# Kernel tuning notes

Measured on AMD Instinct MI355X. Metric: run time of the kernel, lower is better.

Reference implementation:

```python
import jax, jax.numpy as jnp
import numpy as np

D_MANIFOLD = 1024
D_FIBER = 512


def setup_inputs() -> dict:
    key = jax.random.key(0)
    ks = jax.random.split(key, 9)
    B, SQ, SK = 4, 4096, 4096
    m_states = jax.random.normal(ks[0], (B, SQ, D_MANIFOLD), dtype=jnp.float32)
    f_states_k = jax.random.normal(ks[1], (B, SK, D_FIBER), dtype=jnp.float32)
    f_states_v = jax.random.normal(ks[2], (B, SK, D_FIBER), dtype=jnp.float32)
    s_q = 1.0 / np.sqrt(D_MANIFOLD)
    s_f = 1.0 / np.sqrt(D_FIBER)
    W_q = jax.random.uniform(ks[3], (D_MANIFOLD, D_FIBER), jnp.float32, -s_q, s_q)
    b_q = jax.random.uniform(ks[4], (D_FIBER,), jnp.float32, -s_q, s_q)
    W_k = jax.random.uniform(ks[5], (D_FIBER, D_FIBER), jnp.float32, -s_f, s_f)
    b_k = jax.random.uniform(ks[6], (D_FIBER,), jnp.float32, -s_f, s_f)
    W_v = jax.random.uniform(ks[7], (D_FIBER, D_FIBER), jnp.float32, -s_f, s_f)
    b_v = jax.random.uniform(ks[8], (D_FIBER,), jnp.float32, -s_f, s_f)
    return {
        "m_states": m_states,
        "f_states_k": f_states_k,
        "f_states_v": f_states_v,
        "W_q": W_q, "b_q": b_q,
        "W_k": W_k, "b_k": b_k,
        "W_v": W_v, "b_v": b_v,
    }


def reference(m_states, f_states_k, f_states_v, W_q, b_q, W_k, b_k, W_v, b_v):
    scale = D_FIBER ** (-0.5)
    Q = jnp.einsum("bsm,md->bsd", m_states, W_q) + b_q   # [B,SQ,Df]
    K = jnp.einsum("btf,fd->btd", f_states_k, W_k) + b_k  # [B,SK,Df]
    V = jnp.einsum("btf,fd->btd", f_states_v, W_v) + b_v  # [B,SK,Df]
    scores = jnp.einsum("bsd,btd->bst", Q, K) * scale     # [B,SQ,SK]
    weights = jax.nn.softmax(scores, axis=-1)
    return jnp.einsum("bst,btd->bsd", weights, V)         # [B,SQ,Df]
```

## Files before the change

### kernel.cpp

```cpp
#include <hip/hip_runtime.h>


typedef __attribute__((ext_vector_type(8)))  short short8;
typedef __attribute__((ext_vector_type(16))) float f32x16;
typedef __attribute__((ext_vector_type(4)))  float float4v;

__device__ __forceinline__ short f2bf(float x){
  unsigned int u = __float_as_uint(x);
  u = (u + 0x7FFFu + ((u >> 16) & 1u)) >> 16;
  return (short)u;
}

__device__ __forceinline__ unsigned cvt_pk_bf16(float a, float b){
  unsigned r;
  asm("v_cvt_pk_bf16_f32 %0, %1, %2" : "=v"(r) : "v"(a), "v"(b));
  return r;
}

__device__ __forceinline__ float fast_exp2(float x){
  float r; asm("v_exp_f32 %0, %1" : "=v"(r) : "v"(x)); return r;
}

__device__ __forceinline__ void bar_lgkm(){
  asm volatile("s_waitcnt lgkmcnt(0)" ::: "memory");
  __builtin_amdgcn_s_barrier();
}

typedef const __attribute__((address_space(1))) unsigned int guint_t;
typedef __attribute__((address_space(3))) unsigned int luint_t;
__device__ __forceinline__ void gl_lds16(const void* g, void* l){
  __builtin_amdgcn_global_load_lds((guint_t*)g, (luint_t*)l, 16, 0, 0);
}

__global__ __launch_bounds__(256) void transpose_cvt_fused(
    const float* __restrict__ Wq, const float* __restrict__ Wk,
    const float* __restrict__ Wv,
    short* __restrict__ WqT, short* __restrict__ WkT, short* __restrict__ WvT)
{
  int idx = blockIdx.x * 256 + threadIdx.x;
  if (idx < 524288){
    int n = idx & 511, k = idx >> 9;
    WqT[(n<<10) + k] = f2bf(Wq[idx]);
  } else if (idx < 786432){
    int j = idx - 524288; int n = j & 511, k = j >> 9;
    WkT[(n<<9) + k] = f2bf(Wk[j]);
  } else {
    int j = idx - 786432; int n = j & 511, k = j >> 9;
    WvT[(n<<9) + k] = f2bf(Wv[j]);
  }
}

__global__ __launch_bounds__(256, 2) void proj_gemm_fused(
    const float* __restrict__ Aq, const float* __restrict__ Ak,
    const float* __restrict__ Av,
    const short* __restrict__ Wq, const short* __restrict__ Wk,
    const short* __restrict__ Wv,
    const float* __restrict__ bq, const float* __restrict__ bk,
    const float* __restrict__ bv,
    short* __restrict__ Cq, short* __restrict__ Ck, short* __restrict__ Cv,
    float scale)
{
  __shared__ char As[8192];
  __shared__ char Bs[65536];
  const int pz = blockIdx.y;
  const float* A    = (pz==0) ? Aq : (pz==1) ? Ak : Av;
  const short* WT   = (pz==0) ? Wq : (pz==1) ? Wk : Wv;
  const float* bias = (pz==0) ? bq : (pz==1) ? bk : bv;
  short* C          = (pz==0) ? Cq : (pz==1) ? Ck : Cv;
  const int K       = (pz==0) ? 1024 : 512;
  const float alpha = (pz==0) ? scale : 1.0f;

  const int tid = threadIdx.x;
  const int wid = tid >> 6, lane = tid & 63;
  const int lo = lane & 31, hi = lane >> 5;
  const int bm = blockIdx.x;
  const char* WTb = (const char*)WT;

  f32x16 acc[2][4];
  #pragma unroll
  for (int i=0;i<2;i++)
    #pragma unroll
    for (int j=0;j<4;j++)
      #pragma unroll
      for (int r=0;r<16;r++) acc[i][j][r] = 0.0f;

  const int srow = tid >> 2, sslot = tid & 3;
  for (int k0 = 0; k0 < K; k0 += 64) {
    #pragma unroll
    for (int i=0;i<16;i++){
      const int rb0 = wid*128 + i*8;
      const int rr = lane >> 3;
      const void* src = WTb + ((size_t)(rb0 + rr)*K + k0)*2
                        + (((lane&7)*16) ^ (rr<<4));
      gl_lds16(src, Bs + rb0*128);
    }
    {
      const float4v* src = (const float4v*)&A[(size_t)(bm*64+srow)*K + k0 + sslot*16];
      float4v f0 = src[0], f1 = src[1], f2 = src[2], f3 = src[3];
      uint4 u0, u1;
      u0.x = cvt_pk_bf16(f0[0], f0[1]);
      u0.y = cvt_pk_bf16(f0[2], f0[3]);
      u0.z = cvt_pk_bf16(f1[0], f1[1]);
      u0.w = cvt_pk_bf16(f1[2], f1[3]);
      u1.x = cvt_pk_bf16(f2[0], f2[1]);
      u1.y = cvt_pk_bf16(f2[2], f2[3]);
      u1.z = cvt_pk_bf16(f3[0], f3[1]);
      u1.w = cvt_pk_bf16(f3[2], f3[3]);
      const int swz = (srow&7)<<4;
      *(uint4*)(As + srow*128 + ((sslot*32)      ^ swz)) = u0;
      *(uint4*)(As + srow*128 + ((sslot*32 + 16) ^ swz)) = u1;
    }
    __syncthreads();
    #pragma unroll
    for (int dc=0; dc<4; dc++){
      short8 af[2], bfr[4];
      #pragma unroll
      for (int mt=0;mt<2;mt++){
        const int ra = mt*32+lo;
        af[mt] = *(const short8*)(As + ra*128 + ((dc*32 + hi*16) ^ ((ra&7)<<4)));
      }
      #pragma unroll
      for (int nt=0;nt<4;nt++){
        const int rb = wid*128 + nt*32 + lo;
        bfr[nt] = *(const short8*)(Bs + rb*128 + ((dc*32 + hi*16) ^ ((rb&7)<<4)));
      }
      #pragma unroll
      for (int mt=0;mt<2;mt++)
        #pragma unroll
        for (int nt=0;nt<4;nt++)
          acc[mt][nt] = __builtin_amdgcn_mfma_f32_32x32x16_bf16(af[mt], bfr[nt], acc[mt][nt], 0, 0, 0);
    }
    __syncthreads();
  }

  char* Cb = (char*)C;
  #pragma unroll
  for (int nt=0;nt<4;nt++){
    const int col = wid*128 + nt*32 + lo;
    const float bv2 = bias[col];
    #pragma unroll
    for (int mt=0;mt<2;mt++){
      const int grow0 = bm*64 + mt*32;
      if (pz == 0){
        #pragma unroll
        for (int r=0;r<16;r++){
          const int t = grow0 + (r&3) + 8*(r>>2) + 4*hi;
          const int d = col;
          const float val = (acc[mt][nt][r] + bv2) * alpha;
          size_t addr = (size_t)(t>>6)*65536
                      + (size_t)((d>>5)*4 + ((d>>4)&1)*2 + ((d>>3)&1))*1024
                      + (size_t)(t&63)*16 + (d&7)*2;
          *(short*)(Cb + addr) = f2bf(val);
        }
      } else if (pz == 1){
        #pragma unroll
        for (int r=0;r<16;r++){
          const int t = grow0 + (r&3) + 8*(r>>2) + 4*hi;
          const int d = col;
          const float val = acc[mt][nt][r] + bv2;
          size_t addr = (size_t)(t>>9)*524288 + (size_t)((t>>5)&15)*32768
                      + (size_t)((d>>5)*2 + ((d>>4)&1))*1024
                      + (size_t)((t&31) + 32*((d>>3)&1))*16 + (d&7)*2;
          *(short*)(Cb + addr) = f2bf(val);
        }
      } else {
        #pragma unroll
        for (int r=0;r<16;r++){
          const int t = grow0 + (r&3) + 8*(r>>2) + 4*hi;
          const int d = col;
          const float val = acc[mt][nt][r] + bv2;
          size_t addr = (size_t)(t>>9)*524288 + (size_t)(d>>6)*65536
                      + (size_t)(((d>>5)&1)*32 + ((t>>4)&31))*1024
                      + (size_t)((d&31) + 32*((t>>3)&1))*16 + (t&7)*2;
          *(short*)(Cb + addr) = f2bf(val);
        }
      }
    }
  }
}

#define PLDS  65536
#define LSUMO 131072
#define ALDS  133120

__global__ __launch_bounds__(512, 2) void attn_fwd(
    const char* __restrict__ Qg, const char* __restrict__ Kf,
    const char* __restrict__ Vf, float* __restrict__ out)
{
  extern __shared__ char smem[];
  float* lsum_lds = (float*)(smem + LSUMO);

  const int tid = threadIdx.x;
  const int w = tid >> 6, lane = tid & 63;
  const int lo = lane & 31, hi = lane >> 5;
  const int wg = ((blockIdx.x & 7) << 5) + (blockIdx.x >> 3);
  const int b = wg >> 6, qt = wg & 63;
  const size_t qrow0 = ((size_t)b << 12) + (size_t)qt*64;

  const int qbase  = hi*1024 + lo*16;
  const int prbase = PLDS + hi*1024 + lo*16;
  const int pwbase = PLDS + (w<<13) + lo*16 + hi*8;

  {
    const char* qsrc = Qg + (size_t)wg*65536;
    #pragma unroll
    for (int i=0;i<8;i++)
      gl_lds16(qsrc + (w*8+i)*1024 + lane*16, smem + (w*8+i)*1024);
  }

  f32x16 oacc[2][2];
  #pragma unroll
  for (int i=0;i<2;i++)
    #pragma unroll
    for (int j=0;j<2;j++)
      #pragma unroll
      for (int r=0;r<16;r++) oacc[i][j][r]=0.f;
  float ls[2] = {0.f, 0.f};

  const char* Kb = Kf + (size_t)b*4194304;
  const char* Vb = Vf + (size_t)b*4194304;
  short8 kfb[2][8], vfb[2][8];

  {
    const char* kbase0 = Kb + (size_t)(2*w)*32768 + (size_t)lane*16;
    #pragma unroll
    for (int kvsub=0;kvsub<2;kvsub++)
      #pragma unroll
      for (int dc2=0;dc2<2;dc2++)
        #pragma unroll
        for (int ks=0;ks<2;ks++)
          kfb[0][kvsub*4+dc2*2+ks] = *(const short8*)(kbase0
              + (size_t)kvsub*32768 + dc2*2048 + ks*1024);
  }
  __syncthreads();

  for (int kvt = 0; kvt < 8; kvt++) {
    const bool last = (kvt == 7);
    const char* kbaseC = Kb + (size_t)kvt*524288 + (size_t)(2*w)*32768 + (size_t)lane*16;
    const char* kbaseN = Kb + (size_t)((kvt+1)&7)*524288 + (size_t)(2*w)*32768 + (size_t)lane*16;
    const char* vbase  = Vb + (size_t)kvt*524288 + (size_t)(w)*65536 + (size_t)lane*16;

    f32x16 sacc[2][2];
    #pragma unroll
    for (int i=0;i<2;i++)
      #pragma unroll
      for (int j=0;j<2;j++)
        #pragma unroll
        for (int r=0;r<16;r++) sacc[i][j][r]=0.f;

    #pragma unroll
    for (int g=0; g<8; g++){
      const int bf = g & 1;
      if (g < 7){
        #pragma unroll
        for (int kvsub=0;kvsub<2;kvsub++)
          #pragma unroll
          for (int dc2=0;dc2<2;dc2++)
            #pragma unroll
            for (int ks=0;ks<2;ks++)
              kfb[bf^1][kvsub*4+dc2*2+ks] = *(const short8*)(kbaseC
                  + (size_t)kvsub*32768 + (2*(g+1)+dc2)*2048 + ks*1024);
      }
      __builtin_amdgcn_s_setprio(1);
      #pragma unroll
      for (int dc2=0;dc2<2;dc2++)
        #pragma unroll
        for (int ks=0;ks<2;ks++){
          const int dch = 2*g + dc2;
          short8 qf[2];
          #pragma unroll
          for (int qs=0;qs<2;qs++)
            qf[qs] = *(const short8*)(smem + qbase + dch*4096 + ks*2048 + qs*512);
          #pragma unroll
          for (int kvsub=0;kvsub<2;kvsub++)
            #pragma unroll
            for (int qs=0;qs<2;qs++)
              sacc[kvsub][qs] = __builtin_amdgcn_mfma_f32_32x32x16_bf16(
                  kfb[bf][kvsub*4+dc2*2+ks], qf[qs], sacc[kvsub][qs], 0, 0, 0);
        }
      __builtin_amdgcn_s_setprio(0);
    }

    #pragma unroll
    for (int dsub=0;dsub<2;dsub++)
      #pragma unroll
      for (int ts=0;ts<4;ts++)
        vfb[0][dsub*4+ts] = *(const short8*)(vbase + (size_t)dsub*32768 + ts*1024);

    #pragma unroll
    for (int kvsub=0;kvsub<2;kvsub++)
      #pragma unroll
      for (int qs=0;qs<2;qs++){
        #pragma unroll
        for (int g4=0; g4<4; g4++){
          float p0 = fast_exp2(sacc[kvsub][qs][4*g4+0]);
          float p1 = fast_exp2(sacc[kvsub][qs][4*g4+1]);
          float p2 = fast_exp2(sacc[kvsub][qs][4*g4+2]);
          float p3 = fast_exp2(sacc[kvsub][qs][4*g4+3]);
          ls[qs] += (p0 + p1) + (p2 + p3);
          uint2 pv;
          pv.x = cvt_pk_bf16(p0, p1);
          pv.y = cvt_pk_bf16(p2, p3);
          *(uint2*)(smem + pwbase + kvsub*4096 + g4*1024 + qs*512) = pv;
        }
      }
    bar_lgkm();

    #pragma unroll
    for (int g=0; g<8; g++){
      const int bf = g & 1;
      if (g < 7){
        #pragma unroll
        for (int dsub=0;dsub<2;dsub++)
          #pragma unroll
          for (int ts=0;ts<4;ts++)
            vfb[bf^1][dsub*4+ts] = *(const short8*)(vbase
                + (size_t)dsub*32768 + ((g+1)*4+ts)*1024);
      }
      __builtin_amdgcn_s_setprio(1);
      #pragma unroll
      for (int ts=0; ts<4; ts++){
        const int tst = g*4 + ts;
        short8 pf[2];
        #pragma unroll
        for (int qs=0;qs<2;qs++)
          pf[qs] = *(const short8*)(smem + prbase + tst*2048 + qs*512);
        #pragma unroll
        for (int dsub=0;dsub<2;dsub++)
          #pragma unroll
          for (int qs=0;qs<2;qs++)
            oacc[dsub][qs] = __builtin_amdgcn_mfma_f32_32x32x16_bf16(
                vfb[bf][dsub*4+ts], pf[qs], oacc[dsub][qs], 0, 0, 0);
      }
      __builtin_amdgcn_s_setprio(0);
    }

    if (!last){
      #pragma unroll
      for (int kvsub=0;kvsub<2;kvsub++)
        #pragma unroll
        for (int dc2=0;dc2<2;dc2++)
          #pragma unroll
          for (int ks=0;ks<2;ks++)
            kfb[0][kvsub*4+dc2*2+ks] = *(const short8*)(kbaseN
                + (size_t)kvsub*32768 + dc2*2048 + ks*1024);
    }
    bar_lgkm();
  }

  ls[0] += __shfl_xor(ls[0], 32);
  ls[1] += __shfl_xor(ls[1], 32);
  if (hi == 0){
    lsum_lds[w*64 + lo]      = ls[0];
    lsum_lds[w*64 + 32 + lo] = ls[1];
  }
  __syncthreads();

  #pragma unroll
  for (int qs=0;qs<2;qs++){
    float l_tot = 0.f;
    #pragma unroll
    for (int wv=0;wv<8;wv++) l_tot += lsum_lds[wv*64 + qs*32 + lo];
    const float inv = 1.0f / l_tot;
    const size_t row = qrow0 + qs*32 + lo;
    #pragma unroll
    for (int dsub=0;dsub<2;dsub++){
      #pragma unroll
      for (int g4=0;g4<4;g4++){
        float4v ov;
        #pragma unroll
        for (int j=0;j<4;j++) ov[j] = oacc[dsub][qs][4*g4+j]*inv;
        *(float4v*)&out[row*512 + w*64 + dsub*32 + g4*8 + hi*4] = ov;
      }
    }
  }
}

extern "C" void kernel_launch(void* const* d_in, const int* in_sizes, int n_in,
                              void* d_out, int out_size, void* d_ws, size_t ws_size,
                              hipStream_t stream)
{
  const float* m_states = (const float*)d_in[0];
  const float* f_k      = (const float*)d_in[1];
  const float* f_v      = (const float*)d_in[2];
  const float* W_q      = (const float*)d_in[3];
  const float* b_q      = (const float*)d_in[4];
  const float* W_k      = (const float*)d_in[5];
  const float* b_k      = (const float*)d_in[6];
  const float* W_v      = (const float*)d_in[7];
  const float* b_v      = (const float*)d_in[8];
  float* out = (float*)d_out;

  char* ws = (char*)d_ws;
  short* WqT = (short*)(ws);
  short* WkT = (short*)(ws + 1048576);
  short* WvT = (short*)(ws + 1048576 + 524288);
  short* Qb  = (short*)(ws + 2097152);
  short* Kfr = Qb + (size_t)16384*512;
  short* Vfr = Kfr + (size_t)16384*512;

  transpose_cvt_fused<<<4096, 256, 0, stream>>>(W_q, W_k, W_v, WqT, WkT, WvT);

  const float scale = 0.044194173824159216f * 1.4426950408889634f;
  proj_gemm_fused<<<dim3(256,3), 256, 0, stream>>>(
      m_states, f_k, f_v, WqT, WkT, WvT, b_q, b_k, b_v,
      Qb, Kfr, Vfr, scale);

  attn_fwd<<<256, 512, ALDS, stream>>>((const char*)Qb, (const char*)Kfr,
                                       (const char*)Vfr, out);
}
```

Before: 196.1 us.

## Store Q and K in fp8 and compute QK^T with fp8 MFMA

The projection kernel now writes Q and K as fp8 (e4m3) in new packed layouts instead of bf16, and the attention kernel computes scores with the 32x32x16 fp8 MFMA. The softmax scale moves out of the Q projection and into the exp2 argument. This halves Q/K memory traffic and LDS use for Q, lowering the kernel's shared-memory allocation. The cost is a large precision loss in the scores, which risks exceeding the accuracy tolerance. The fp8 MFMA may also not be faster per instruction for this shape.

```diff
diff --git a/kernel.cpp b/kernel.cpp
--- a/kernel.cpp
+++ b/kernel.cpp
@@ -4,6 +4,8 @@
 typedef __attribute__((ext_vector_type(8)))  short short8;
 typedef __attribute__((ext_vector_type(16))) float f32x16;
 typedef __attribute__((ext_vector_type(4)))  float float4v;
+
+#define SC_QK (0.044194173824159216f * 1.4426950408889634f)
 
 __device__ __forceinline__ short f2bf(float x){
   unsigned int u = __float_as_uint(x);
@@ -15,6 +17,11 @@
   unsigned r;
   asm("v_cvt_pk_bf16_f32 %0, %1, %2" : "=v"(r) : "v"(a), "v"(b));
   return r;
+}
+
+__device__ __forceinline__ unsigned char f2fp8(float x){
+  int p = __builtin_amdgcn_cvt_pk_fp8_f32(x, 0.f, 0, false);
+  return (unsigned char)(p & 0xFF);
 }
 
 __device__ __forceinline__ float fast_exp2(float x){
@@ -57,8 +64,7 @@
     const short* __restrict__ Wv,
     const float* __restrict__ bq, const float* __restrict__ bk,
     const float* __restrict__ bv,
-    short* __restrict__ Cq, short* __restrict__ Ck, short* __restrict__ Cv,
-    float scale)
+    char* __restrict__ Cq, char* __restrict__ Ck, char* __restrict__ Cv)
 {
   __shared__ char As[8192];
   __shared__ char Bs[65536];
@@ -66,9 +72,8 @@
   const float* A    = (pz==0) ? Aq : (pz==1) ? Ak : Av;
   const short* WT   = (pz==0) ? Wq : (pz==1) ? Wk : Wv;
   const float* bias = (pz==0) ? bq : (pz==1) ? bk : bv;
-  short* C          = (pz==0) ? Cq : (pz==1) ? Ck : Cv;
+  char* Cb          = (pz==0) ? Cq : (pz==1) ? Ck : Cv;
   const int K       = (pz==0) ? 1024 : 512;
-  const float alpha = (pz==0) ? scale : 1.0f;
 
   const int tid = threadIdx.x;
   const int wid = tid >> 6, lane = tid & 63;
@@ -133,7 +138,6 @@
     __syncthreads();
   }
 
-  char* Cb = (char*)C;
   #pragma unroll
   for (int nt=0;nt<4;nt++){
     const int col = wid*128 + nt*32 + lo;
@@ -146,11 +150,10 @@
         for (int r=0;r<16;r++){
           const int t = grow0 + (r&3) + 8*(r>>2) + 4*hi;
           const int d = col;
-          const float val = (acc[mt][nt][r] + bv2) * alpha;
-          size_t addr = (size_t)(t>>6)*65536
-                      + (size_t)((d>>5)*4 + ((d>>4)&1)*2 + ((d>>3)&1))*1024
-                      + (size_t)(t&63)*16 + (d&7)*2;
-          *(short*)(Cb + addr) = f2bf(val);
+          const float val = acc[mt][nt][r] + bv2;
+          size_t addr = (size_t)(t>>6)*32768 + (size_t)(d>>3)*512
+                      + (size_t)(t&63)*8 + (d&7);
+          *(unsigned char*)(Cb + addr) = f2fp8(val);
         }
       } else if (pz == 1){
         #pragma unroll
@@ -158,10 +161,10 @@
           const int t = grow0 + (r&3) + 8*(r>>2) + 4*hi;
           const int d = col;
           const float val = acc[mt][nt][r] + bv2;
-          size_t addr = (size_t)(t>>9)*524288 + (size_t)((t>>5)&15)*32768
-                      + (size_t)((d>>5)*2 + ((d>>4)&1))*1024
-                      + (size_t)((t&31) + 32*((d>>3)&1))*16 + (d&7)*2;
-          *(short*)(Cb + addr) = f2bf(val);
+          size_t addr = (size_t)(t>>9)*262144 + (size_t)((t>>5)&15)*16384
+                      + (size_t)(d>>4)*512
+                      + (size_t)((t&31) + 32*((d>>3)&1))*8 + (d&7);
+          *(unsigned char*)(Cb + addr) = f2fp8(val);
         }
       } else {
         #pragma unroll
@@ -179,9 +182,9 @@
   }
 }
 
-#define PLDS  65536
-#define LSUMO 131072
-#define ALDS  133120
+#define PLDS  32768
+#define LSUMO 98304
+#define ALDS  100352
 
 __global__ __launch_bounds__(512, 2) void attn_fwd(
     const char* __restrict__ Qg, const char* __restrict__ Kf,
@@ -197,15 +200,15 @@
   const int b = wg >> 6, qt = wg & 63;
   const size_t qrow0 = ((size_t)b << 12) + (size_t)qt*64;
 
-  const int qbase  = hi*1024 + lo*16;
+  const int qbase  = hi*512 + lo*8;
   const int prbase = PLDS + hi*1024 + lo*16;
   const int pwbase = PLDS + (w<<13) + lo*16 + hi*8;
 
   {
-    const char* qsrc = Qg + (size_t)wg*65536;
-    #pragma unroll
-    for (int i=0;i<8;i++)
-      gl_lds16(qsrc + (w*8+i)*1024 + lane*16, smem + (w*8+i)*1024);
+    const char* qsrc = Qg + (size_t)wg*32768;
+    #pragma unroll
+    for (int i=0;i<4;i++)
+      gl_lds16(qsrc + (w*4+i)*1024 + lane*16, smem + (w*4+i)*1024);
   }
 
   f32x16 oacc[2][2];
@@ -217,27 +220,28 @@
       for (int r=0;r<16;r++) oacc[i][j][r]=0.f;
   float ls[2] = {0.f, 0.f};
 
-  const char* Kb = Kf + (size_t)b*4194304;
+  const char* Kb = Kf + (size_t)b*2097152;
   const char* Vb = Vf + (size_t)b*4194304;
-  short8 kfb[2][8], vfb[2][8];
+  long   kfb[2][8];
+  short8 vfb[2][8];
 
   {
-    const char* kbase0 = Kb + (size_t)(2*w)*32768 + (size_t)lane*16;
+    const char* kbase0 = Kb + (size_t)(2*w)*16384 + (size_t)lane*8;
     #pragma unroll
     for (int kvsub=0;kvsub<2;kvsub++)
       #pragma unroll
       for (int dc2=0;dc2<2;dc2++)
         #pragma unroll
         for (int ks=0;ks<2;ks++)
-          kfb[0][kvsub*4+dc2*2+ks] = *(const short8*)(kbase0
-              + (size_t)kvsub*32768 + dc2*2048 + ks*1024);
+          kfb[0][kvsub*4+dc2*2+ks] = *(const long*)(kbase0
+              + (size_t)kvsub*16384 + dc2*1024 + ks*512);
   }
   __syncthreads();
 
   for (int kvt = 0; kvt < 8; kvt++) {
     const bool last = (kvt == 7);
-    const char* kbaseC = Kb + (size_t)kvt*524288 + (size_t)(2*w)*32768 + (size_t)lane*16;
-    const char* kbaseN = Kb + (size_t)((kvt+1)&7)*524288 + (size_t)(2*w)*32768 + (size_t)lane*16;
+    const char* kbaseC = Kb + (size_t)kvt*262144 + (size_t)(2*w)*16384 + (size_t)lane*8;
+    const char* kbaseN = Kb + (size_t)((kvt+1)&7)*262144 + (size_t)(2*w)*16384 + (size_t)lane*8;
     const char* vbase  = Vb + (size_t)kvt*524288 + (size_t)(w)*65536 + (size_t)lane*16;
 
     f32x16 sacc[2][2];
@@ -258,8 +262,8 @@
           for (int dc2=0;dc2<2;dc2++)
             #pragma unroll
             for (int ks=0;ks<2;ks++)
-              kfb[bf^1][kvsub*4+dc2*2+ks] = *(const short8*)(kbaseC
-                  + (size_t)kvsub*32768 + (2*(g+1)+dc2)*2048 + ks*1024);
+              kfb[bf^1][kvsub*4+dc2*2+ks] = *(const long*)(kbaseC
+                  + (size_t)kvsub*16384 + (2*(g+1)+dc2)*1024 + ks*512);
       }
       __builtin_amdgcn_s_setprio(1);
       #pragma unroll
@@ -267,15 +271,15 @@
         #pragma unroll
         for (int ks=0;ks<2;ks++){
           const int dch = 2*g + dc2;
-          short8 qf[2];
+          long qf[2];
           #pragma unroll
           for (int qs=0;qs<2;qs++)
-            qf[qs] = *(const short8*)(smem + qbase + dch*4096 + ks*2048 + qs*512);
+            qf[qs] = *(const long*)(smem + qbase + dch*2048 + ks*1024 + qs*256);
           #pragma unroll
           for (int kvsub=0;kvsub<2;kvsub++)
             #pragma unroll
             for (int qs=0;qs<2;qs++)
-              sacc[kvsub][qs] = __builtin_amdgcn_mfma_f32_32x32x16_bf16(
+              sacc[kvsub][qs] = __builtin_amdgcn_mfma_f32_32x32x16_fp8_fp8(
                   kfb[bf][kvsub*4+dc2*2+ks], qf[qs], sacc[kvsub][qs], 0, 0, 0);
         }
       __builtin_amdgcn_s_setprio(0);
@@ -293,10 +297,10 @@
       for (int qs=0;qs<2;qs++){
         #pragma unroll
         for (int g4=0; g4<4; g4++){
-          float p0 = fast_exp2(sacc[kvsub][qs][4*g4+0]);
-          float p1 = fast_exp2(sacc[kvsub][qs][4*g4+1]);
-          float p2 = fast_exp2(sacc[kvsub][qs][4*g4+2]);
-          float p3 = fast_exp2(sacc[kvsub][qs][4*g4+3]);
+          float p0 = fast_exp2(sacc[kvsub][qs][4*g4+0] * SC_QK);
+          float p1 = fast_exp2(sacc[kvsub][qs][4*g4+1] * SC_QK);
+          float p2 = fast_exp2(sacc[kvsub][qs][4*g4+2] * SC_QK);
+          float p3 = fast_exp2(sacc[kvsub][qs][4*g4+3] * SC_QK);
           ls[qs] += (p0 + p1) + (p2 + p3);
           uint2 pv;
           pv.x = cvt_pk_bf16(p0, p1);
@@ -342,8 +346,8 @@
         for (int dc2=0;dc2<2;dc2++)
           #pragma unroll
           for (int ks=0;ks<2;ks++)
-            kfb[0][kvsub*4+dc2*2+ks] = *(const short8*)(kbaseN
-                + (size_t)kvsub*32768 + dc2*2048 + ks*1024);
+            kfb[0][kvsub*4+dc2*2+ks] = *(const long*)(kbaseN
+                + (size_t)kvsub*16384 + dc2*1024 + ks*512);
     }
     bar_lgkm();
   }
@@ -395,17 +399,15 @@
   short* WqT = (short*)(ws);
   short* WkT = (short*)(ws + 1048576);
   short* WvT = (short*)(ws + 1048576 + 524288);
-  short* Qb  = (short*)(ws + 2097152);
-  short* Kfr = Qb + (size_t)16384*512;
-  short* Vfr = Kfr + (size_t)16384*512;
+  char*  Qb  = ws + 2097152;
+  char*  Kfr = Qb + 8388608;
+  char*  Vfr = Kfr + 8388608;
 
   transpose_cvt_fused<<<4096, 256, 0, stream>>>(W_q, W_k, W_v, WqT, WkT, WvT);
 
-  const float scale = 0.044194173824159216f * 1.4426950408889634f;
   proj_gemm_fused<<<dim3(256,3), 256, 0, stream>>>(
       m_states, f_k, f_v, WqT, WkT, WvT, b_q, b_k, b_v,
-      Qb, Kfr, Vfr, scale);
-
-  attn_fwd<<<256, 512, ALDS, stream>>>((const char*)Qb, (const char*)Kfr,
-                                       (const char*)Vfr, out);
-}
+      Qb, Kfr, Vfr);
+
+  attn_fwd<<<256, 512, ALDS, stream>>>(Qb, Kfr, Vfr, out);
+}
```

After: 181.8 us. -7.3%, faster.
